# Kernel tuning notes

Hardware: AMD Instinct MI355X
Metric: run time of the kernel (lower is better)

Reference implementation:

```python
import jax, jax.numpy as jnp
import numpy as np

EPS = 1e-15


def _trace(t):
    return jnp.einsum('bii->b', t)


def _ortho_loss(ss, k):
    n = jnp.linalg.norm(ss, axis=(-1, -2), keepdims=True)
    diff = ss / n - jnp.eye(k, dtype=ss.dtype) / np.float32(np.sqrt(k))
    return jnp.mean(jnp.linalg.norm(diff, axis=(-1, -2)))


def _mincut_terms(s, adj):
    out_adj = jnp.einsum('bnk,bnm,bml->bkl', s, adj, s)
    d_flat = adj.sum(-1)  # degrees [B,N]
    num = _trace(out_adj)
    den = _trace(jnp.einsum('bnk,bn,bnl->bkl', s, d_flat, s)) + EPS
    return out_adj, num, den, d_flat


def dense_mincut_rewiring(x, adj, s, mask):
    k = s.shape[-1]  # 2
    m = mask[..., None].astype(x.dtype)
    s = jax.nn.softmax(s, axis=-1) * m
    _, num, den, _ = _mincut_terms(s, adj)
    mincut_loss = -jnp.mean(num / den)
    ortho_loss = _ortho_loss(jnp.einsum('bnk,bnl->bkl', s, s), k)
    # laplacian derivative of spectral gap wrt A_uv: (f_u - f_v)^2, f = soft bipartition
    f = s[..., 0]
    dlam = (f[:, :, None] - f[:, None, :]) ** 2
    return adj * (1.0 - dlam), mincut_loss, ortho_loss


def dense_CT_rewiring(x, adj, s, mask):
    k = s.shape[-1]
    m = mask[..., None].astype(x.dtype)
    s = jax.nn.softmax(s, axis=-1) * m
    d_flat = adj.sum(-1)
    sds = _trace(jnp.einsum('bnk,bn,bnl->bkl', s, d_flat, s))
    sas = _trace(jnp.einsum('bnk,bnm,bml->bkl', s, adj, s))
    den = _trace(jnp.einsum('bnk,bnl->bkl', s, s)) + EPS
    ct_loss = jnp.mean((sds - sas) / den)  # tr(Z^T L Z) / tr(Z^T Z)
    ortho_loss = _ortho_loss(jnp.einsum('bnk,bnl->bkl', s, s), k)
    # pairwise CT distances ||z_u - z_v|| / vol(G), sparsified by A
    sq = (s * s).sum(-1)
    d2 = sq[:, :, None] + sq[:, None, :] - 2.0 * jnp.einsum('bnk,bmk->bnm', s, s)
    ct_dist = jnp.sqrt(jnp.maximum(d2, 0.0) + 1e-12)
    vol = d_flat.sum(-1)
    new_adj = (ct_dist / (vol[:, None, None] + EPS)) * adj
    return new_adj, ct_loss, ortho_loss


def dense_mincut_pool(x, adj, s, mask):
    k = s.shape[-1]
    m = mask[..., None].astype(x.dtype)
    s = jax.nn.softmax(s, axis=-1) * m
    x = x * m
    out = jnp.einsum('bnk,bnf->bkf', s, x)
    out_adj, num, den, _ = _mincut_terms(s, adj)
    mincut_loss = -jnp.mean(num / den)
    ortho_loss = _ortho_loss(jnp.einsum('bnk,bnl->bkl', s, s), k)
    out_adj = out_adj * (1.0 - jnp.eye(k, dtype=adj.dtype))  # zero diagonal
    d = jnp.sqrt(out_adj.sum(-1)) + EPS  # [B,k]
    out_adj = out_adj / d[:, None, :] / d[:, :, None]
    return out, out_adj, mincut_loss, ortho_loss


def _dgc(x, adj, w_rel, b_rel, w_root):
    # DenseGraphConv(aggr='add'): lin_rel(A @ x) + lin_root(x)
    return jnp.matmul(adj, x) @ w_rel + b_rel + x @ w_root


def setup_inputs() -> dict:
    B, N, IN, H, KC, OUT, KMC = 16, 1024, 128, 32, 32, 10, 16
    keys = iter(jax.random.split(jax.random.key(0), 48))

    def lin(fin, fout):
        lim = float(1.0 / np.sqrt(fin))
        return (jax.random.uniform(next(keys), (fin, fout), jnp.float32, -lim, lim),
                jax.random.uniform(next(keys), (fout,), jnp.float32, -lim, lim))

    x = jax.random.normal(next(keys), (B, N, IN), jnp.float32)
    u = jax.random.uniform(next(keys), (B, N, N), jnp.float32)
    a = (u < 0.0156).astype(jnp.float32)  # avg degree ~16
    adj = jnp.maximum(a, jnp.swapaxes(a, 1, 2)) * (1.0 - jnp.eye(N, dtype=jnp.float32))
    mask = jnp.ones((B, N), dtype=bool)
    W1, b1 = lin(IN, H)
    Wrw, brw = lin(H, 2)
    Wg_rel, bg = lin(H, H); Wg_root, _ = lin(H, H)
    Wmcg, bmcg = lin(H, KMC)
    W2g_rel, b2g = lin(H, H); W2g_root, _ = lin(H, H)
    Wct, bct = lin(H, KC)
    Wc_rel, bc = lin(H, H); Wc_root, _ = lin(H, H)
    Wmcc, bmcc = lin(H, KMC)
    Wcat, bcat = lin(2 * H, H)
    W2, b2 = lin(H, H)
    W3, b3 = lin(H, OUT)
    return dict(x=x, adj=adj, mask=mask, W1=W1, b1=b1, Wrw=Wrw, brw=brw,
                Wg_rel=Wg_rel, bg=bg, Wg_root=Wg_root, Wmcg=Wmcg, bmcg=bmcg,
                W2g_rel=W2g_rel, b2g=b2g, W2g_root=W2g_root, Wct=Wct, bct=bct,
                Wc_rel=Wc_rel, bc=bc, Wc_root=Wc_root, Wmcc=Wmcc, bmcc=bmcc,
                Wcat=Wcat, bcat=bcat, W2=W2, b2=b2, W3=W3, b3=b3)


def reference(x, adj, mask, W1, b1, Wrw, brw, Wg_rel, bg, Wg_root, Wmcg, bmcg,
              W2g_rel, b2g, W2g_root, Wct, bct, Wc_rel, bc, Wc_root, Wmcc, bmcc,
              Wcat, bcat, W2, b2, W3, b3):
    x = x @ W1 + b1
    # GAP branch
    adj_gap, mc_rw, ol_rw = dense_mincut_rewiring(x, adj, x @ Wrw + brw, mask)
    x_gap = _dgc(x, adj_gap, Wg_rel, bg, Wg_root)
    x_gap, adj_gap, mc1, ol1 = dense_mincut_pool(x_gap, adj_gap, x_gap @ Wmcg + bmcg, mask)
    x_gap = _dgc(x_gap, adj_gap, W2g_rel, b2g, W2g_root)
    # CT branch
    adj_ct, ct_loss, ol_ct = dense_CT_rewiring(x, adj, x @ Wct + bct, mask)
    x_ct = _dgc(x, adj_ct, Wc_rel, bc, Wc_root)
    x_ct, adj_ct, mc2, ol2 = dense_mincut_pool(x_ct, adj_ct, x_ct @ Wmcc + bmcc, mask)
    x_ct = _dgc(x_ct, adj_ct, W2g_rel, b2g, W2g_root)  # source reuses self.conv2gap here
    h = jax.nn.relu(jnp.concatenate([x_gap, x_ct], axis=2) @ Wcat + bcat).sum(axis=1)
    h = jax.nn.relu(h @ W2 + b2)
    logits = h @ W3 + b3
    main_loss = mc_rw + ct_loss + mc1 + mc2
    ortho_loss = ol_rw + ol_ct + ol1 + ol2
    return (jax.nn.log_softmax(logits, axis=-1), main_loss, ortho_loss)
```

## Files before the change

### kernel.cpp

```cpp
#include <hip/hip_runtime.h>
#include <math.h>

#define BB   16
#define NNODE 1024
#define INF_ 128
#define HH   32
#define KMC  16
#define CAP  128
#define EPS15 1e-15f

typedef float v4f __attribute__((ext_vector_type(4)));

#define OFF_X      0
#define OFF_SRW    524288
#define OFF_SQCT   557056
#define OFF_SCT    573440
#define OFF_D      1097728
#define OFF_NUMRW  1114112
#define OFF_SAS    1130496
#define OFF_DGAP   1146880
#define OFF_DCT    1163264
#define OFF_XGAP   2228224
#define OFF_XCT    2752512
#define OFF_S2G    3276800
#define OFF_S2C    3538944
#define OFF_FROB   4325376
#define OFF_VOL    4325888
#define OFF_OUTG   4326032
#define OFF_OUTC   4334224
#define OFF_G2G    4342416
#define OFF_G2C    4346512
#define OFF_OAG    4350608
#define OFF_OAC    4354704
#define OFF_ENNZ   4358800
#define OFF_EIDX   4375184
#define OFF_EWG    5423760
#define OFF_EWC    7520912
#define OFF_PACK   9618064
#define OFF_BSUM   9683600

__device__ __forceinline__ float wave_sum(float v) {
#pragma unroll
  for (int off = 32; off >= 1; off >>= 1) v += __shfl_xor(v, off, 64);
  return v;
}

__device__ __forceinline__ void wave_sum4(float& a, float& b, float& c, float& d) {
#pragma unroll
  for (int off = 32; off >= 1; off >>= 1) {
    a += __shfl_xor(a, off, 64);
    b += __shfl_xor(b, off, 64);
    c += __shfl_xor(c, off, 64);
    d += __shfl_xor(d, off, 64);
  }
}

__device__ __forceinline__ void team_reduce_f4(float4& a) {
#pragma unroll
  for (int off = 4; off <= 32; off <<= 1) {
    a.x += __shfl_xor(a.x, off, 64);
    a.y += __shfl_xor(a.y, off, 64);
    a.z += __shfl_xor(a.z, off, 64);
    a.w += __shfl_xor(a.w, off, 64);
  }
}

__device__ __forceinline__ float blk_sum(float v, float* sred, int tid) {
  v = wave_sum(v);
  __syncthreads();
  if ((tid & 63) == 0) sred[tid >> 6] = v;
  __syncthreads();
  return sred[0] + sred[1] + sred[2] + sred[3];
}

__device__ __forceinline__ void blk_sum5(float* v, float (*sm)[4], int tid) {
  int w = tid >> 6, lane = tid & 63;
#pragma unroll
  for (int i = 0; i < 5; i++) {
#pragma unroll
    for (int off = 32; off >= 1; off >>= 1) v[i] += __shfl_xor(v[i], off, 64);
  }
  if (lane == 0) {
#pragma unroll
    for (int i = 0; i < 5; i++) sm[i][w] = v[i];
  }
  __syncthreads();
#pragma unroll
  for (int i = 0; i < 5; i++) v[i] = sm[i][0] + sm[i][1] + sm[i][2] + sm[i][3];
}

__global__ __launch_bounds__(256) void k_fused0(
    const float* __restrict__ adj, const float* __restrict__ x,
    const float* __restrict__ W1, const float* __restrict__ b1,
    const float* __restrict__ Wrw, const float* __restrict__ brw,
    const float* __restrict__ Wct, const float* __restrict__ bct,
    float* __restrict__ ws)
{
  __shared__ __align__(16) float sW1[INF_*HH];
  __shared__ __align__(16) float sWct[HH*HH];
  __shared__ float sWrw[HH*2];
  __shared__ float sb1[HH], sbct[HH], sbrw[2];
  __shared__ __align__(16) float sx[8*INF_];
  __shared__ float sX[8*HH];
  __shared__ unsigned int s_e32[4][4][CAP/2];
  int tid = threadIdx.x;
  if (blockIdx.x < 1024) {
    int w = tid >> 6, lane = tid & 63;
    int row0 = blockIdx.x * 16 + w * 4;
    v4f v[16];
#pragma unroll
    for (int rr = 0; rr < 4; rr++) {
      const v4f* ar = (const v4f*)(adj + (size_t)(row0 + rr) * NNODE);
#pragma unroll
      for (int it = 0; it < 4; it++)
        v[rr*4 + it] = __builtin_nontemporal_load(&ar[it*64 + lane]);
    }
#pragma unroll
    for (int rr = 0; rr < 4; rr++) {
      int row = row0 + rr;
      int c = 0;
#pragma unroll
      for (int it = 0; it < 4; it++) {
        v4f a4 = v[rr*4 + it];
        c += (a4.x != 0.f) + (a4.y != 0.f) + (a4.z != 0.f) + (a4.w != 0.f);
      }
      int p = c;
#pragma unroll
      for (int off = 1; off < 64; off <<= 1) {
        int t = __shfl_up(p, off, 64);
        if (lane >= off) p += t;
      }
      int excl = p - c;
      int total = __shfl(p, 63, 64);
      unsigned short* es = (unsigned short*)s_e32[w][rr];
      int pos = excl;
#pragma unroll
      for (int it = 0; it < 4; it++) {
        v4f a4 = v[rr*4 + it];
        int m0 = it*256 + lane*4;
        if (a4.x != 0.f) { if (pos < CAP) es[pos] = (unsigned short)(m0+0); pos++; }
        if (a4.y != 0.f) { if (pos < CAP) es[pos] = (unsigned short)(m0+1); pos++; }
        if (a4.z != 0.f) { if (pos < CAP) es[pos] = (unsigned short)(m0+2); pos++; }
        if (a4.w != 0.f) { if (pos < CAP) es[pos] = (unsigned short)(m0+3); pos++; }
      }
      int nnzc = total < CAP ? total : CAP;
      __syncthreads();
      unsigned int* dst = (unsigned int*)((unsigned short*)(ws + OFF_EIDX) + (size_t)row*CAP);
      int n32 = (nnzc + 1) >> 1;
      if (lane < n32) dst[lane] = s_e32[w][rr][lane];
      if (lane == 0) {
        ((int*)(ws + OFF_ENNZ))[row] = nnzc;
        ws[OFF_D + row] = (float)total;
      }
    }
  } else {
    for (int i = tid; i < INF_*HH/4; i += 256)
      ((float4*)sW1)[i] = ((const float4*)W1)[i];
    ((float4*)sWct)[tid] = ((const float4*)Wct)[tid];
    if (tid < HH*2) sWrw[tid] = Wrw[tid];
    if (tid < HH) { sb1[tid] = b1[tid]; sbct[tid] = bct[tid]; }
    if (tid < 2) sbrw[tid] = brw[tid];
    size_t row0 = (size_t)(blockIdx.x - 1024) * 8;
    ((float4*)sx)[tid] = ((const float4*)(x + row0 * INF_))[tid];
    __syncthreads();
    int r = tid >> 5, h = tid & 31;
    float acc = sb1[h];
#pragma unroll 8
    for (int k = 0; k < INF_; k++) acc += sx[r*INF_ + k] * sW1[k*HH + h];
    size_t row = row0 + r;
    ws[OFF_X + row*HH + h] = acc;
    sX[r*HH + h] = acc;
    __syncthreads();
    float sraw = sbct[h];
#pragma unroll
    for (int k = 0; k < HH; k++) sraw += sX[r*HH + k] * sWct[k*HH + h];
    float mx = sraw;
#pragma unroll
    for (int off = 16; off >= 1; off >>= 1) mx = fmaxf(mx, __shfl_xor(mx, off, 32));
    float e = __expf(sraw - mx);
    float sum = e;
#pragma unroll
    for (int off = 16; off >= 1; off >>= 1) sum += __shfl_xor(sum, off, 32);
    float sv = e / sum;
    ws[OFF_SCT + row*HH + h] = sv;
    float sq = sv * sv;
#pragma unroll
    for (int off = 16; off >= 1; off >>= 1) sq += __shfl_xor(sq, off, 32);
    float xv = sX[r*HH + h];
    float t0 = xv * sWrw[h*2 + 0];
    float t1 = xv * sWrw[h*2 + 1];
#pragma unroll
    for (int off = 16; off >= 1; off >>= 1) { t0 += __shfl_xor(t0, off, 32); t1 += __shfl_xor(t1, off, 32); }
    if (h == 0) {
      ws[OFF_SQCT + row] = sq;
      float r0 = t0 + sbrw[0], r1 = t1 + sbrw[1];
      float m2 = fmaxf(r0, r1);
      float e0 = __expf(r0 - m2), e1 = __expf(r1 - m2);
      float inv = 1.0f / (e0 + e1);
      float s0 = e0*inv, s1 = e1*inv;
      ((float2*)(ws + OFF_SRW))[row] = make_float2(s0, s1);
      ((float4*)(ws + OFF_PACK))[row] = make_float4(s0, s1, sq, 0.f);
    }
  }
}

__global__ __launch_bounds__(256) void k_edgefeat(
    const float* __restrict__ Wg_rel, const float* __restrict__ bg, const float* __restrict__ Wg_root,
    const float* __restrict__ Wc_rel, const float* __restrict__ bc, const float* __restrict__ Wc_root,
    const float* __restrict__ Wmcg, const float* __restrict__ bmcg,
    const float* __restrict__ Wmcc, const float* __restrict__ bmcc,
    float* __restrict__ out, float* __restrict__ ws)
{
  __shared__ float sp[8][32];
  __shared__ float sred[4];
  __shared__ __align__(16) float sWgrel[HH*HH], sWgroot[HH*HH], sWcrel[HH*HH], sWcroot[HH*HH];
  __shared__ float sbg[HH], sbc[HH];
  __shared__ __align__(16) float sYg[4*HH], sYc[4*HH];
  __shared__ float sXr[4*HH], sxg[4*HH], sxc[4*HH];
  int tid = threadIdx.x;
  if (blockIdx.x < 4096) {
    int xcd = blockIdx.x & 7;
    int idx = blockIdx.x >> 3;
    int b = xcd*2 + (idx >> 8);
    int chunk = idx & 255;
    int base4 = b*NNODE + chunk*4;
    ((float4*)sWgrel)[tid]  = ((const float4*)Wg_rel)[tid];
    ((float4*)sWgroot)[tid] = ((const float4*)Wg_root)[tid];
    ((float4*)sWcrel)[tid]  = ((const float4*)Wc_rel)[tid];
    ((float4*)sWcroot)[tid] = ((const float4*)Wc_root)[tid];
    if (tid < HH)  { sbg[tid] = bg[tid]; sbc[tid] = bc[tid]; }
    if (tid < 128) sXr[tid] = ws[OFF_X + (size_t)base4*HH + tid];
    float vp = 0.f;
#pragma unroll
    for (int i = 0; i < 4; i++) vp += ws[OFF_D + (size_t)b*NNODE + tid + i*256];

    const float* X = ws + OFF_X;
    const float2* srw = (const float2*)(ws + OFF_SRW);
    const float* sqct = ws + OFF_SQCT;
    const float* sct = ws + OFF_SCT;
    const float4* pack = (const float4*)(ws + OFF_PACK) + (size_t)b*NNODE;
    int w = tid >> 6, lane = tid & 63;
    int tm = lane & 3;
    int row = base4 + w;
    int nnz = ((const int*)(ws + OFF_ENNZ))[row];
    const unsigned short* eidx = (const unsigned short*)(ws + OFF_EIDX) + (size_t)row*CAP;
    const float4* cn4 = (const float4*)(sct + (size_t)row * HH);
    float4 c0 = cn4[tm*2], c1 = cn4[tm*2 + 1];
    float2 srwn = srw[row];
    float f_n = srwn.x;
    float sq_n = sqct[row];
    float numrw_p = 0.f, sas_p = 0.f, dg_p = 0.f, dc_p = 0.f;
    float4 yg0 = make_float4(0,0,0,0), yg1 = make_float4(0,0,0,0);
    float4 yc0 = make_float4(0,0,0,0), yc1 = make_float4(0,0,0,0);
    for (int e = (lane >> 2); e < nnz; e += 16) {
      int m = eidx[e];
      size_t mo = ((size_t)b*NNODE + m);
      const float4* cm4 = (const float4*)(sct + mo * HH);
      const float4* xm4 = (const float4*)(X + mo * HH);
      float4 d0 = cm4[tm*2], d1 = cm4[tm*2 + 1];
      float4 x0 = xm4[tm*2], x1 = xm4[tm*2 + 1];
      float4 pk = pack[m];
      float dot = c0.x*d0.x + c0.y*d0.y + c0.z*d0.z + c0.w*d0.w
                + c1.x*d1.x + c1.y*d1.y + c1.z*d1.z + c1.w*d1.w;
      dot += __shfl_xor(dot, 1, 64);
      dot += __shfl_xor(dot, 2, 64);
      numrw_p += srwn.x*pk.x + srwn.y*pk.y;
      float df = f_n - pk.x;
      float wg = 1.0f - df*df;
      float d2 = sq_n + pk.z - 2.0f*dot;
      float wc = sqrtf(fmaxf(d2, 0.0f) + 1e-12f);
      sas_p += dot;
      dg_p += wg;
      dc_p += wc;
      yg0.x += wg*x0.x; yg0.y += wg*x0.y; yg0.z += wg*x0.z; yg0.w += wg*x0.w;
      yg1.x += wg*x1.x; yg1.y += wg*x1.y; yg1.z += wg*x1.z; yg1.w += wg*x1.w;
      yc0.x += wc*x0.x; yc0.y += wc*x0.y; yc0.z += wc*x0.z; yc0.w += wc*x0.w;
      yc1.x += wc*x1.x; yc1.y += wc*x1.y; yc1.z += wc*x1.z; yc1.w += wc*x1.w;
      if (tm == 0) {
        size_t eo = (size_t)row*CAP + e;
        ws[OFF_EWG + eo] = wg;
        ws[OFF_EWC + eo] = wc;
      }
    }
    wave_sum4(numrw_p, sas_p, dg_p, dc_p);
    if (lane == 0) {
      ws[OFF_NUMRW + row] = numrw_p * 0.25f;
      ws[OFF_SAS + row] = sas_p * 0.25f;
      ws[OFF_DGAP + row] = dg_p * 0.25f;
      ws[OFF_DCT + row] = dc_p * 0.25f;
    }
    team_reduce_f4(yg0); team_reduce_f4(yg1);
    team_reduce_f4(yc0); team_reduce_f4(yc1);
    if (lane < 4) {
      ((float4*)&sYg[w*HH + tm*8])[0] = yg0;
      ((float4*)&sYg[w*HH + tm*8])[1] = yg1;
      ((float4*)&sYc[w*HH + tm*8])[0] = yc0;
      ((float4*)&sYc[w*HH + tm*8])[1] = yc1;
    }
    float vol = blk_sum(vp, sred, tid);
    float ivol = 1.0f / (vol + EPS15);
    {
      int r = tid >> 6;
      int h = (tid >> 1) & 31;
      int half = tid & 1;
      int kb = half * 16;
      float accg = 0.f, accg2 = 0.f, accc = 0.f, accc2 = 0.f;
#pragma unroll
      for (int kk = 0; kk < 16; kk++) {
        int k = kb + kk;
        float ygv = sYg[r*HH + k], Xv = sXr[r*HH + k], ycv = sYc[r*HH + k];
        accg  += ygv * sWgrel[k*HH + h];
        accg2 += Xv  * sWgroot[k*HH + h];
        accc  += ycv * sWcrel[k*HH + h];
        accc2 += Xv  * sWcroot[k*HH + h];
      }
      accg  += __shfl_xor(accg, 1, 64);
      accg2 += __shfl_xor(accg2, 1, 64);
      accc  += __shfl_xor(accc, 1, 64);
      accc2 += __shfl_xor(accc2, 1, 64);
      if (half == 0) {
        float xgv = sbg[h] + accg + accg2;
        float xcv = sbc[h] + ivol*accc + accc2;
        size_t rw = (size_t)base4 + r;
        ws[OFF_XGAP + rw*HH + h] = xgv;
        ws[OFF_XCT  + rw*HH + h] = xcv;
        sxg[r*HH + h] = xgv;
        sxc[r*HH + h] = xcv;
      }
    }
    __syncthreads();
    if (tid < 128) {
      int r = tid >> 5, h = tid & 31;
      int j = h & 15, halfsel = h >> 4;
      const float* sin_ = halfsel ? sxc : sxg;
      const float* sw = halfsel ? Wmcc : Wmcg;
      float raw = halfsel ? bmcc[j] : bmcg[j];
#pragma unroll
      for (int k = 0; k < HH; k++) raw += sin_[r*HH + k] * sw[k*KMC + j];
      float mx = raw;
#pragma unroll
      for (int off = 8; off >= 1; off >>= 1) mx = fmaxf(mx, __shfl_xor(mx, off, 16));
      float e = __expf(raw - mx);
      float sum = e;
#pragma unroll
      for (int off = 8; off >= 1; off >>= 1) sum += __shfl_xor(sum, off, 16);
      float sv = e / sum;
      size_t rw = (size_t)base4 + r;
      if (halfsel == 0) ws[OFF_S2G + rw*KMC + j] = sv;
      else              ws[OFF_S2C + rw*KMC + j] = sv;
    }
  } else if (blockIdx.x < 4608) {
    int blk = blockIdx.x - 4096;
    int xcd = blk & 7;
    int idx = blk >> 3;
    int b = xcd*2 + (idx >> 5);
    int i = idx & 31;
    const float* sct = ws + OFF_SCT + (size_t)b*NNODE*HH;
    int j = tid & 31, seg = tid >> 5;
    float acc = 0.f;
    for (int n = seg*128; n < seg*128 + 128; n++)
      acc += sct[n*HH + i] * sct[n*HH + j];
    sp[seg][j] = acc;
    __syncthreads();
    if (tid < 32) {
      float g = 0.f;
#pragma unroll
      for (int s = 0; s < 8; s++) g += sp[s][tid];
      float p = g * g;
#pragma unroll
      for (int off = 16; off >= 1; off >>= 1) p += __shfl_xor(p, off, 32);
      if (tid == 0) ws[OFF_FROB + b*32 + i] = p;
    }
  } else {
    int b = blockIdx.x - 4608;
    if (b == 0 && tid < 2) out[160 + tid] = 0.f;
    if (tid < 12) ws[OFF_BSUM + b*12 + tid] = 0.f;
    for (int i = tid; i < 2048; i += 256) ws[OFF_OUTG + b*2048 + i] = 0.f;
    float vp = 0.f;
    for (int n = tid; n < NNODE; n += 256) vp += ws[OFF_D + (size_t)b*NNODE + n];
    float vol = blk_sum(vp, sred, tid);
    if (tid == 0) ws[OFF_VOL + b] = vol;
  }
}

__global__ __launch_bounds__(512) void k_passred(float* __restrict__ ws)
{
  __shared__ float sg[32*16], sc[32*16], stg[32*16], stc[32*16];
  __shared__ float sxg[32*32], sxc[32*32];
  int xcd = blockIdx.x & 7;
  int idx = blockIdx.x >> 3;
  int b = xcd*2 + (idx >> 5);
  int chunk = idx & 31;
  int tid = threadIdx.x;
  size_t n0 = (size_t)b * NNODE + chunk * 32;
  const float* pG  = ws + OFF_S2G  + n0 * KMC;
  const float* pC  = ws + OFF_S2C  + n0 * KMC;
  const float* pXG = ws + OFF_XGAP + n0 * HH;
  const float* pXC = ws + OFF_XCT  + n0 * HH;
  sg[tid] = pG[tid];
  sc[tid] = pC[tid];
  sxg[tid] = pXG[tid]; sxg[tid + 512] = pXG[tid + 512];
  sxc[tid] = pXC[tid]; sxc[tid + 512] = pXC[tid + 512];
  {
    int r = tid >> 4, k = tid & 15;
    size_t row = n0 + r;
    int nnz = ((const int*)(ws + OFF_ENNZ))[row];
    const unsigned short* eidx = (const unsigned short*)(ws + OFF_EIDX) + row * CAP;
    const float* ewg = ws + OFF_EWG + row * CAP;
    const float* ewc = ws + OFF_EWC + row * CAP;
    const float* S2G = ws + OFF_S2G + (size_t)b * NNODE * KMC;
    const float* S2C = ws + OFF_S2C + (size_t)b * NNODE * KMC;
    float ag = 0.f, ac = 0.f;
    int e = 0;
    for (; e + 1 < nnz; e += 2) {
      int m0 = eidx[e], m1 = eidx[e + 1];
      float g0 = ewg[e], g1 = ewg[e + 1];
      float c0 = ewc[e], c1 = ewc[e + 1];
      ag += g0 * S2G[(size_t)m0 * KMC + k] + g1 * S2G[(size_t)m1 * KMC + k];
      ac += c0 * S2C[(size_t)m0 * KMC + k] + c1 * S2C[(size_t)m1 * KMC + k];
    }
    if (e < nnz) {
      int m = eidx[e];
      ag += ewg[e] * S2G[(size_t)m * KMC + k];
      ac += ewc[e] * S2C[(size_t)m * KMC + k];
    }
    stg[r * 16 + k] = ag;
    stc[r * 16 + k] = ac;
  }
  __syncthreads();
  int sub = tid >> 8, t = tid & 255;
  { int k0 = t >> 5, h0 = t & 31;
    float og0 = 0.f, og1 = 0.f, oc0 = 0.f, oc1 = 0.f;
#pragma unroll
    for (int i = 0; i < 16; i++) {
      int r = sub * 16 + i;
      float xgv = sxg[r*32 + h0], xcv = sxc[r*32 + h0];
      og0 += sg[r*16 + k0]     * xgv;
      og1 += sg[r*16 + k0 + 8] * xgv;
      oc0 += sc[r*16 + k0]     * xcv;
      oc1 += sc[r*16 + k0 + 8] * xcv;
    }
    atomicAdd(&ws[OFF_OUTG + b*512 + k0*32 + h0],     og0);
    atomicAdd(&ws[OFF_OUTG + b*512 + (k0+8)*32 + h0], og1);
    atomicAdd(&ws[OFF_OUTC + b*512 + k0*32 + h0],     oc0);
    atomicAdd(&ws[OFF_OUTC + b*512 + (k0+8)*32 + h0], oc1);
  }
  { int kk = t >> 4, l = t & 15;
    float gg = 0.f, gc = 0.f, ag = 0.f, ac = 0.f;
#pragma unroll
    for (int i = 0; i < 16; i++) {
      int r = sub * 16 + i;
      float sgk = sg[r*16 + kk], sck = sc[r*16 + kk];
      gg += sgk * sg [r*16 + l];
      gc += sck * sc [r*16 + l];
      ag += sgk * stg[r*16 + l];
      ac += sck * stc[r*16 + l];
    }
    atomicAdd(&ws[OFF_G2G + b*256 + t], gg);
    atomicAdd(&ws[OFF_G2C + b*256 + t], gc);
    atomicAdd(&ws[OFF_OAG + b*256 + t], ag);
    atomicAdd(&ws[OFF_OAC + b*256 + t], ac);
  }
  if (tid < 32) {
    size_t gn = n0 + tid;
    float ng = 0.f, nc = 0.f;
#pragma unroll
    for (int j = 0; j < KMC; j++) {
      float a = sg[tid*16 + j], c2 = sc[tid*16 + j];
      ng += a*a; nc += c2*c2;
    }
    float dgv = ws[OFF_DGAP + gn];
    float dcv = ws[OFF_DCT + gn];
    float d   = ws[OFF_D + gn];
    float2 s  = ((const float2*)(ws + OFF_SRW))[gn];
    float sq  = ws[OFF_SQCT + gn];
    float nmr = ws[OFF_NUMRW + gn];
    float sasv= ws[OFF_SAS + gn];
    float u0 = dgv*ng, u1 = dcv*nc, u2 = ng, u3 = nc;
    float u4 = d*(s.x*s.x + s.y*s.y), u5 = nmr, u6 = d*sq, u7 = sasv;
    float u8 = sq, u9 = s.x*s.x, u10 = s.x*s.y, u11 = s.y*s.y;
#pragma unroll
    for (int off = 16; off >= 1; off >>= 1) {
      u0 += __shfl_xor(u0, off, 32);  u1 += __shfl_xor(u1, off, 32);
      u2 += __shfl_xor(u2, off, 32);  u3 += __shfl_xor(u3, off, 32);
      u4 += __shfl_xor(u4, off, 32);  u5 += __shfl_xor(u5, off, 32);
      u6 += __shfl_xor(u6, off, 32);  u7 += __shfl_xor(u7, off, 32);
      u8 += __shfl_xor(u8, off, 32);  u9 += __shfl_xor(u9, off, 32);
      u10 += __shfl_xor(u10, off, 32); u11 += __shfl_xor(u11, off, 32);
    }
    if (tid == 0) {
      float* bs = ws + OFF_BSUM + b*12;
      atomicAdd(bs + 0, u0);  atomicAdd(bs + 1, u1);  atomicAdd(bs + 2, u2);
      atomicAdd(bs + 3, u3);  atomicAdd(bs + 4, u4);  atomicAdd(bs + 5, u5);
      atomicAdd(bs + 6, u6);  atomicAdd(bs + 7, u7);  atomicAdd(bs + 8, u8);
      atomicAdd(bs + 9, u9);  atomicAdd(bs + 10, u10); atomicAdd(bs + 11, u11);
    }
  }
}

__global__ __launch_bounds__(256) void k_batch2(
    const float* __restrict__ W2g_rel, const float* __restrict__ b2g, const float* __restrict__ W2g_root,
    const float* __restrict__ Wcat, const float* __restrict__ bcat,
    const float* __restrict__ W2, const float* __restrict__ b2,
    const float* __restrict__ W3, const float* __restrict__ b3,
    float* __restrict__ out, float* __restrict__ ws)
{
  __shared__ float sOAg[256], sOAc[256], sOutg[512], sOutc[512];
  __shared__ float sW2grel[1024], sW2groot[1024], sWcat[2048], sW2l[1024];
  __shared__ float sPg[512], sPc[512], sXg2[512], sXc2[512], sHt[512];
  __shared__ float sHs[32], sH2[32], sLg[16], sScal[2];
  __shared__ float sdkg[16], sdkc[16];
  __shared__ float smm[5][4];
  int b = blockIdx.x, tid = threadIdx.x;
  sOAg[tid] = ws[OFF_OAG + b*256 + tid];
  sOAc[tid] = ws[OFF_OAC + b*256 + tid];
  sOutg[tid]       = ws[OFF_OUTG + b*512 + tid];
  sOutg[tid + 256] = ws[OFF_OUTG + b*512 + tid + 256];
  sOutc[tid]       = ws[OFF_OUTC + b*512 + tid];
  sOutc[tid + 256] = ws[OFF_OUTC + b*512 + tid + 256];
  for (int i = tid; i < 1024; i += 256) { sW2grel[i] = W2g_rel[i]; sW2groot[i] = W2g_root[i]; sW2l[i] = W2[i]; }
  for (int i = tid; i < 2048; i += 256) sWcat[i] = Wcat[i];
  float v[5];
  v[0] = (tid < 32) ? ws[OFF_FROB + b*32 + tid] : 0.f;
  float gv = ws[OFF_G2G + b*256 + tid];
  float cv = ws[OFF_G2C + b*256 + tid];
  v[1] = gv*gv; v[2] = cv*cv;
  __syncthreads();
  v[3] = (tid < 16) ? sOAg[tid*17] : 0.f;
  v[4] = (tid < 16) ? sOAc[tid*17] : 0.f;
  blk_sum5(v, smm, tid);
  float frob2 = v[0], frobg2 = v[1], frobc2 = v[2], num1 = v[3], num2u = v[4];
  float vol = ws[OFF_VOL + b];
  float ivol = 1.0f / (vol + EPS15);
  if (tid == 0) {
    const float* bs = ws + OFF_BSUM + b*12;
    float den1 = bs[0], den2u = bs[1], trg = bs[2], trc = bs[3];
    float denrw = bs[4], num = bs[5], sds = bs[6], sas = bs[7], denct = bs[8];
    float g00 = bs[9], g01 = bs[10], g11 = bs[11];
    float mcrw = -num / (denrw + EPS15);
    float ctb  = (sds - sas) / (denct + EPS15);
    float nrw = sqrtf(g00*g00 + 2.f*g01*g01 + g11*g11);
    float olrw = sqrtf(fmaxf(2.f - 2.f*(g00 + g11)/(nrw*1.41421356237f), 0.f));
    float nct = sqrtf(frob2);
    float olct = sqrtf(fmaxf(2.f - 2.f*denct/(nct*5.65685424949f), 0.f));
    float mc1 = -num1 / (den1 + EPS15);
    float mc2 = -(num2u*ivol) / (den2u*ivol + EPS15);
    float ol1 = sqrtf(fmaxf(2.f - 2.f*trg/(sqrtf(frobg2)*4.f), 0.f));
    float ol2 = sqrtf(fmaxf(2.f - 2.f*trc/(sqrtf(frobc2)*4.f), 0.f));
    atomicAdd(out + 160, (mcrw + ctb + mc1 + mc2) * 0.0625f);
    atomicAdd(out + 161, (olrw + olct + ol1 + ol2) * 0.0625f);
  }
  sOAc[tid] *= ivol;
  __syncthreads();
  if (tid < 16) { sOAg[tid*17] = 0.f; sOAc[tid*17] = 0.f; }
  __syncthreads();
  if (tid < 16) {
    float rg = 0.f, rc = 0.f;
#pragma unroll
    for (int l = 0; l < 16; l++) { rg += sOAg[tid*16 + l]; rc += sOAc[tid*16 + l]; }
    sdkg[tid] = sqrtf(rg) + EPS15;
    sdkc[tid] = sqrtf(rc) + EPS15;
  }
  __syncthreads();
  { int k = tid >> 4, l = tid & 15;
    sOAg[tid] /= (sdkg[k]*sdkg[l]);
    sOAc[tid] /= (sdkc[k]*sdkc[l]); }
  __syncthreads();
  { int k = tid >> 5, h = tid & 31;
    float p0 = 0, p1 = 0, q0 = 0, q1 = 0;
#pragma unroll
    for (int l = 0; l < 16; l++) {
      p0 += sOAg[k*16 + l] * sOutg[l*32 + h];
      p1 += sOAg[(k+8)*16 + l] * sOutg[l*32 + h];
      q0 += sOAc[k*16 + l] * sOutc[l*32 + h];
      q1 += sOAc[(k+8)*16 + l] * sOutc[l*32 + h];
    }
    sPg[k*32 + h] = p0; sPg[(k+8)*32 + h] = p1;
    sPc[k*32 + h] = q0; sPc[(k+8)*32 + h] = q1;
  }
  __syncthreads();
  { int k = tid >> 5, h = tid & 31;
    float bb2 = b2g[h];
    float a0 = bb2, a1 = bb2, c0 = bb2, c1 = bb2;
#pragma unroll
    for (int q = 0; q < 32; q++) {
      float wr = sW2grel[q*32 + h], wo = sW2groot[q*32 + h];
      a0 += sPg[k*32 + q]*wr + sOutg[k*32 + q]*wo;
      a1 += sPg[(k+8)*32 + q]*wr + sOutg[(k+8)*32 + q]*wo;
      c0 += sPc[k*32 + q]*wr + sOutc[k*32 + q]*wo;
      c1 += sPc[(k+8)*32 + q]*wr + sOutc[(k+8)*32 + q]*wo;
    }
    sXg2[k*32 + h] = a0; sXg2[(k+8)*32 + h] = a1;
    sXc2[k*32 + h] = c0; sXc2[(k+8)*32 + h] = c1;
  }
  __syncthreads();
  { int k = tid >> 5, h = tid & 31;
    float bb = bcat[h];
    float t0 = bb, t1 = bb;
#pragma unroll
    for (int q = 0; q < 32; q++) {
      float w1v = sWcat[q*32 + h], w2v = sWcat[(q+32)*32 + h];
      t0 += sXg2[k*32 + q]*w1v + sXc2[k*32 + q]*w2v;
      t1 += sXg2[(k+8)*32 + q]*w1v + sXc2[(k+8)*32 + q]*w2v;
    }
    sHt[k*32 + h] = fmaxf(t0, 0.f);
    sHt[(k+8)*32 + h] = fmaxf(t1, 0.f);
  }
  __syncthreads();
  if (tid < 32) {
    float s = 0.f;
#pragma unroll
    for (int k = 0; k < 16; k++) s += sHt[k*32 + tid];
    sHs[tid] = s;
  }
  __syncthreads();
  if (tid < 32) {
    float a = b2[tid];
#pragma unroll
    for (int q = 0; q < 32; q++) a += sHs[q]*sW2l[q*32 + tid];
    sH2[tid] = fmaxf(a, 0.f);
  }
  __syncthreads();
  if (tid < 10) {
    float a = b3[tid];
#pragma unroll
    for (int q = 0; q < 32; q++) a += sH2[q]*W3[q*10 + tid];
    sLg[tid] = a;
  }
  __syncthreads();
  if (tid == 0) {
    float m = sLg[0];
    for (int o = 1; o < 10; o++) m = fmaxf(m, sLg[o]);
    float se = 0.f;
    for (int o = 0; o < 10; o++) se += __expf(sLg[o] - m);
    sScal[0] = m; sScal[1] = logf(se);
  }
  __syncthreads();
  if (tid < 10) out[b*10 + tid] = sLg[tid] - sScal[0] - sScal[1];
}

extern "C" void kernel_launch(void* const* d_in, const int* in_sizes, int n_in,
                              void* d_out, int out_size, void* d_ws, size_t ws_size,
                              hipStream_t stream)
{
  const float* x       = (const float*)d_in[0];
  const float* adj     = (const float*)d_in[1];
  const float* W1      = (const float*)d_in[3];
  const float* b1      = (const float*)d_in[4];
  const float* Wrw     = (const float*)d_in[5];
  const float* brw     = (const float*)d_in[6];
  const float* Wg_rel  = (const float*)d_in[7];
  const float* bg      = (const float*)d_in[8];
  const float* Wg_root = (const float*)d_in[9];
  const float* Wmcg    = (const float*)d_in[10];
  const float* bmcg    = (const float*)d_in[11];
  const float* W2g_rel = (const float*)d_in[12];
  const float* b2g     = (const float*)d_in[13];
  const float* W2g_root= (const float*)d_in[14];
  const float* Wct     = (const float*)d_in[15];
  const float* bct     = (const float*)d_in[16];
  const float* Wc_rel  = (const float*)d_in[17];
  const float* bc      = (const float*)d_in[18];
  const float* Wc_root = (const float*)d_in[19];
  const float* Wmcc    = (const float*)d_in[20];
  const float* bmcc    = (const float*)d_in[21];
  const float* Wcat    = (const float*)d_in[22];
  const float* bcat    = (const float*)d_in[23];
  const float* W2      = (const float*)d_in[24];
  const float* b2      = (const float*)d_in[25];
  const float* W3      = (const float*)d_in[26];
  const float* b3      = (const float*)d_in[27];
  float* out = (float*)d_out;
  float* ws  = (float*)d_ws;

  k_fused0<<<dim3(3072), dim3(256), 0, stream>>>(adj, x, W1, b1, Wrw, brw, Wct, bct, ws);
  k_edgefeat<<<dim3(4624), dim3(256), 0, stream>>>(Wg_rel, bg, Wg_root, Wc_rel, bc, Wc_root,
                                                   Wmcg, bmcg, Wmcc, bmcc, out, ws);
  k_passred<<<dim3(512), dim3(512), 0, stream>>>(ws);
  k_batch2<<<dim3(16), dim3(256), 0, stream>>>(W2g_rel, b2g, W2g_root, Wcat, bcat,
                                               W2, b2, W3, b3, out, ws);
}
```

Baseline: 248.0 us.

## Process four rows per wave in edge-feature kernel, drop shared weight staging

The edge-feature kernel now has each wave loop over four rows, so a block covers 16 rows and the grid shrinks from 4096 to 1024 blocks for that part. The per-block staging of four 32x32 weight matrices into shared memory and the block-wide volume reduction are removed. Weights are read directly from global or L2, the volume is reduced per wave, and the dense projection and softmax run wave-locally without block barriers. This amortizes per-block setup and synchronization, at the cost of fewer blocks, less parallelism and repeated uncached global weight reads.

```diff
diff --git a/kernel.cpp b/kernel.cpp
--- a/kernel.cpp
+++ b/kernel.cpp
@@ -213,144 +213,141 @@
 {
   __shared__ float sp[8][32];
   __shared__ float sred[4];
-  __shared__ __align__(16) float sWgrel[HH*HH], sWgroot[HH*HH], sWcrel[HH*HH], sWcroot[HH*HH];
-  __shared__ float sbg[HH], sbc[HH];
-  __shared__ __align__(16) float sYg[4*HH], sYc[4*HH];
-  __shared__ float sXr[4*HH], sxg[4*HH], sxc[4*HH];
+  __shared__ __align__(16) float sY[4][2][HH];
+  __shared__ __align__(16) float sXw[4][HH];
+  __shared__ float sxgw[4][HH], sxcw[4][HH];
   int tid = threadIdx.x;
-  if (blockIdx.x < 4096) {
+  if (blockIdx.x < 1024) {
     int xcd = blockIdx.x & 7;
     int idx = blockIdx.x >> 3;
-    int b = xcd*2 + (idx >> 8);
-    int chunk = idx & 255;
-    int base4 = b*NNODE + chunk*4;
-    ((float4*)sWgrel)[tid]  = ((const float4*)Wg_rel)[tid];
-    ((float4*)sWgroot)[tid] = ((const float4*)Wg_root)[tid];
-    ((float4*)sWcrel)[tid]  = ((const float4*)Wc_rel)[tid];
-    ((float4*)sWcroot)[tid] = ((const float4*)Wc_root)[tid];
-    if (tid < HH)  { sbg[tid] = bg[tid]; sbc[tid] = bc[tid]; }
-    if (tid < 128) sXr[tid] = ws[OFF_X + (size_t)base4*HH + tid];
-    float vp = 0.f;
-#pragma unroll
-    for (int i = 0; i < 4; i++) vp += ws[OFF_D + (size_t)b*NNODE + tid + i*256];
-
+    int b = xcd*2 + (idx >> 6);
+    int chunk = idx & 63;
+    int base16 = b*NNODE + chunk*16;
+    int w = tid >> 6, lane = tid & 63;
+    int tm = lane & 3;
+    int h = lane & 31, half = lane >> 5;
+    int j = lane & 15, gsel = (lane >> 4) & 1;
     const float* X = ws + OFF_X;
+    const float* sct = ws + OFF_SCT;
     const float2* srw = (const float2*)(ws + OFF_SRW);
     const float* sqct = ws + OFF_SQCT;
-    const float* sct = ws + OFF_SCT;
     const float4* pack = (const float4*)(ws + OFF_PACK) + (size_t)b*NNODE;
-    int w = tid >> 6, lane = tid & 63;
-    int tm = lane & 3;
-    int row = base4 + w;
-    int nnz = ((const int*)(ws + OFF_ENNZ))[row];
-    const unsigned short* eidx = (const unsigned short*)(ws + OFF_EIDX) + (size_t)row*CAP;
-    const float4* cn4 = (const float4*)(sct + (size_t)row * HH);
-    float4 c0 = cn4[tm*2], c1 = cn4[tm*2 + 1];
-    float2 srwn = srw[row];
-    float f_n = srwn.x;
-    float sq_n = sqct[row];
-    float numrw_p = 0.f, sas_p = 0.f, dg_p = 0.f, dc_p = 0.f;
-    float4 yg0 = make_float4(0,0,0,0), yg1 = make_float4(0,0,0,0);
-    float4 yc0 = make_float4(0,0,0,0), yc1 = make_float4(0,0,0,0);
-    for (int e = (lane >> 2); e < nnz; e += 16) {
-      int m = eidx[e];
-      size_t mo = ((size_t)b*NNODE + m);
-      const float4* cm4 = (const float4*)(sct + mo * HH);
-      const float4* xm4 = (const float4*)(X + mo * HH);
-      float4 d0 = cm4[tm*2], d1 = cm4[tm*2 + 1];
-      float4 x0 = xm4[tm*2], x1 = xm4[tm*2 + 1];
-      float4 pk = pack[m];
-      float dot = c0.x*d0.x + c0.y*d0.y + c0.z*d0.z + c0.w*d0.w
-                + c1.x*d1.x + c1.y*d1.y + c1.z*d1.z + c1.w*d1.w;
-      dot += __shfl_xor(dot, 1, 64);
-      dot += __shfl_xor(dot, 2, 64);
-      numrw_p += srwn.x*pk.x + srwn.y*pk.y;
-      float df = f_n - pk.x;
-      float wg = 1.0f - df*df;
-      float d2 = sq_n + pk.z - 2.0f*dot;
-      float wc = sqrtf(fmaxf(d2, 0.0f) + 1e-12f);
-      sas_p += dot;
-      dg_p += wg;
-      dc_p += wc;
-      yg0.x += wg*x0.x; yg0.y += wg*x0.y; yg0.z += wg*x0.z; yg0.w += wg*x0.w;
-      yg1.x += wg*x1.x; yg1.y += wg*x1.y; yg1.z += wg*x1.z; yg1.w += wg*x1.w;
-      yc0.x += wc*x0.x; yc0.y += wc*x0.y; yc0.z += wc*x0.z; yc0.w += wc*x0.w;
-      yc1.x += wc*x1.x; yc1.y += wc*x1.y; yc1.z += wc*x1.z; yc1.w += wc*x1.w;
-      if (tm == 0) {
-        size_t eo = (size_t)row*CAP + e;
-        ws[OFF_EWG + eo] = wg;
-        ws[OFF_EWC + eo] = wc;
-      }
-    }
-    wave_sum4(numrw_p, sas_p, dg_p, dc_p);
-    if (lane == 0) {
-      ws[OFF_NUMRW + row] = numrw_p * 0.25f;
-      ws[OFF_SAS + row] = sas_p * 0.25f;
-      ws[OFF_DGAP + row] = dg_p * 0.25f;
-      ws[OFF_DCT + row] = dc_p * 0.25f;
-    }
-    team_reduce_f4(yg0); team_reduce_f4(yg1);
-    team_reduce_f4(yc0); team_reduce_f4(yc1);
-    if (lane < 4) {
-      ((float4*)&sYg[w*HH + tm*8])[0] = yg0;
-      ((float4*)&sYg[w*HH + tm*8])[1] = yg1;
-      ((float4*)&sYc[w*HH + tm*8])[0] = yc0;
-      ((float4*)&sYc[w*HH + tm*8])[1] = yc1;
-    }
-    float vol = blk_sum(vp, sred, tid);
-    float ivol = 1.0f / (vol + EPS15);
-    {
-      int r = tid >> 6;
-      int h = (tid >> 1) & 31;
-      int half = tid & 1;
-      int kb = half * 16;
-      float accg = 0.f, accg2 = 0.f, accc = 0.f, accc2 = 0.f;
-#pragma unroll
-      for (int kk = 0; kk < 16; kk++) {
-        int k = kb + kk;
-        float ygv = sYg[r*HH + k], Xv = sXr[r*HH + k], ycv = sYc[r*HH + k];
-        accg  += ygv * sWgrel[k*HH + h];
-        accg2 += Xv  * sWgroot[k*HH + h];
-        accc  += ycv * sWcrel[k*HH + h];
-        accc2 += Xv  * sWcroot[k*HH + h];
-      }
-      accg  += __shfl_xor(accg, 1, 64);
-      accg2 += __shfl_xor(accg2, 1, 64);
-      accc  += __shfl_xor(accc, 1, 64);
-      accc2 += __shfl_xor(accc2, 1, 64);
-      if (half == 0) {
-        float xgv = sbg[h] + accg + accg2;
-        float xcv = sbc[h] + ivol*accc + accc2;
-        size_t rw = (size_t)base4 + r;
-        ws[OFF_XGAP + rw*HH + h] = xgv;
-        ws[OFF_XCT  + rw*HH + h] = xcv;
-        sxg[r*HH + h] = xgv;
-        sxc[r*HH + h] = xcv;
-      }
-    }
-    __syncthreads();
-    if (tid < 128) {
-      int r = tid >> 5, h = tid & 31;
-      int j = h & 15, halfsel = h >> 4;
-      const float* sin_ = halfsel ? sxc : sxg;
-      const float* sw = halfsel ? Wmcc : Wmcg;
-      float raw = halfsel ? bmcc[j] : bmcg[j];
-#pragma unroll
-      for (int k = 0; k < HH; k++) raw += sin_[r*HH + k] * sw[k*KMC + j];
-      float mx = raw;
-#pragma unroll
-      for (int off = 8; off >= 1; off >>= 1) mx = fmaxf(mx, __shfl_xor(mx, off, 16));
-      float e = __expf(raw - mx);
-      float sum = e;
-#pragma unroll
-      for (int off = 8; off >= 1; off >>= 1) sum += __shfl_xor(sum, off, 16);
-      float sv = e / sum;
-      size_t rw = (size_t)base4 + r;
-      if (halfsel == 0) ws[OFF_S2G + rw*KMC + j] = sv;
-      else              ws[OFF_S2C + rw*KMC + j] = sv;
-    }
-  } else if (blockIdx.x < 4608) {
-    int blk = blockIdx.x - 4096;
+    float bgv = bg[h], bcv = bc[h];
+    float bmv = gsel ? bmcc[j] : bmcg[j];
+    const float* Wmc = gsel ? Wmcc : Wmcg;
+    float vp = 0.f;
+#pragma unroll
+    for (int i = 0; i < 16; i++) vp += ws[OFF_D + (size_t)b*NNODE + lane + i*64];
+    float ivol = 1.0f / (wave_sum(vp) + EPS15);
+
+    for (int rr = 0; rr < 4; rr++) {
+      int row = base16 + w*4 + rr;
+      int nnz = ((const int*)(ws + OFF_ENNZ))[row];
+      const unsigned short* eidx = (const unsigned short*)(ws + OFF_EIDX) + (size_t)row*CAP;
+      const float4* cn4 = (const float4*)(sct + (size_t)row * HH);
+      float4 c0 = cn4[tm*2], c1 = cn4[tm*2 + 1];
+      if (lane < 8) ((float4*)sXw[w])[lane] = ((const float4*)(X + (size_t)row * HH))[lane];
+      float2 srwn = srw[row];
+      float f_n = srwn.x;
+      float sq_n = sqct[row];
+      float numrw_p = 0.f, sas_p = 0.f, dg_p = 0.f, dc_p = 0.f;
+      float4 yg0 = make_float4(0,0,0,0), yg1 = make_float4(0,0,0,0);
+      float4 yc0 = make_float4(0,0,0,0), yc1 = make_float4(0,0,0,0);
+      for (int e = (lane >> 2); e < nnz; e += 16) {
+        int m = eidx[e];
+        size_t mo = ((size_t)b*NNODE + m);
+        const float4* cm4 = (const float4*)(sct + mo * HH);
+        const float4* xm4 = (const float4*)(X + mo * HH);
+        float4 d0 = cm4[tm*2], d1 = cm4[tm*2 + 1];
+        float4 x0 = xm4[tm*2], x1 = xm4[tm*2 + 1];
+        float4 pk = pack[m];
+        float dot = c0.x*d0.x + c0.y*d0.y + c0.z*d0.z + c0.w*d0.w
+                  + c1.x*d1.x + c1.y*d1.y + c1.z*d1.z + c1.w*d1.w;
+        dot += __shfl_xor(dot, 1, 64);
+        dot += __shfl_xor(dot, 2, 64);
+        numrw_p += srwn.x*pk.x + srwn.y*pk.y;
+        float df = f_n - pk.x;
+        float wg = 1.0f - df*df;
+        float d2 = sq_n + pk.z - 2.0f*dot;
+        float wc = sqrtf(fmaxf(d2, 0.0f) + 1e-12f);
+        sas_p += dot;
+        dg_p += wg;
+        dc_p += wc;
+        yg0.x += wg*x0.x; yg0.y += wg*x0.y; yg0.z += wg*x0.z; yg0.w += wg*x0.w;
+        yg1.x += wg*x1.x; yg1.y += wg*x1.y; yg1.z += wg*x1.z; yg1.w += wg*x1.w;
+        yc0.x += wc*x0.x; yc0.y += wc*x0.y; yc0.z += wc*x0.z; yc0.w += wc*x0.w;
+        yc1.x += wc*x1.x; yc1.y += wc*x1.y; yc1.z += wc*x1.z; yc1.w += wc*x1.w;
+        if (tm == 0) {
+          size_t eo = (size_t)row*CAP + e;
+          ws[OFF_EWG + eo] = wg;
+          ws[OFF_EWC + eo] = wc;
+        }
+      }
+      wave_sum4(numrw_p, sas_p, dg_p, dc_p);
+      if (lane == 0) {
+        ws[OFF_NUMRW + row] = numrw_p * 0.25f;
+        ws[OFF_SAS + row] = sas_p * 0.25f;
+        ws[OFF_DGAP + row] = dg_p * 0.25f;
+        ws[OFF_DCT + row] = dc_p * 0.25f;
+      }
+      team_reduce_f4(yg0); team_reduce_f4(yg1);
+      team_reduce_f4(yc0); team_reduce_f4(yc1);
+      if (lane < 4) {
+        ((float4*)&sY[w][0][tm*8])[0] = yg0;
+        ((float4*)&sY[w][0][tm*8])[1] = yg1;
+        ((float4*)&sY[w][1][tm*8])[0] = yc0;
+        ((float4*)&sY[w][1][tm*8])[1] = yc1;
+      }
+      {
+        float accg = 0.f, accg2 = 0.f, accc = 0.f, accc2 = 0.f;
+#pragma unroll
+        for (int kk = 0; kk < 16; kk++) {
+          int k = half*16 + kk;
+          float ygv = sY[w][0][k], Xv = sXw[w][k], ycv = sY[w][1][k];
+          accg  += ygv * Wg_rel[k*HH + h];
+          accg2 += Xv  * Wg_root[k*HH + h];
+          accc  += ycv * Wc_rel[k*HH + h];
+          accc2 += Xv  * Wc_root[k*HH + h];
+        }
+        accg  += __shfl_xor(accg, 32, 64);
+        accg2 += __shfl_xor(accg2, 32, 64);
+        accc  += __shfl_xor(accc, 32, 64);
+        accc2 += __shfl_xor(accc2, 32, 64);
+        float xgv = bgv + accg + accg2;
+        float xcv = bcv + ivol*accc + accc2;
+        if (half == 0) {
+          ws[OFF_XGAP + (size_t)row*HH + h] = xgv;
+          ws[OFF_XCT  + (size_t)row*HH + h] = xcv;
+          sxgw[w][h] = xgv;
+          sxcw[w][h] = xcv;
+        }
+      }
+      {
+        const float* xin = gsel ? sxcw[w] : sxgw[w];
+        float raw = 0.f;
+#pragma unroll
+        for (int kk = 0; kk < 16; kk++) {
+          int k = half*16 + kk;
+          raw += xin[k] * Wmc[k*KMC + j];
+        }
+        raw += __shfl_xor(raw, 32, 64);
+        raw += bmv;
+        float mx = raw;
+#pragma unroll
+        for (int off = 8; off >= 1; off >>= 1) mx = fmaxf(mx, __shfl_xor(mx, off, 64));
+        float e = __expf(raw - mx);
+        float sum = e;
+#pragma unroll
+        for (int off = 8; off >= 1; off >>= 1) sum += __shfl_xor(sum, off, 64);
+        float sv = e / sum;
+        if (half == 0) {
+          if (gsel == 0) ws[OFF_S2G + (size_t)row*KMC + j] = sv;
+          else           ws[OFF_S2C + (size_t)row*KMC + j] = sv;
+        }
+      }
+    }
+  } else if (blockIdx.x < 1536) {
+    int blk = blockIdx.x - 1024;
     int xcd = blk & 7;
     int idx = blk >> 3;
     int b = xcd*2 + (idx >> 5);
@@ -372,7 +369,7 @@
       if (tid == 0) ws[OFF_FROB + b*32 + i] = p;
     }
   } else {
-    int b = blockIdx.x - 4608;
+    int b = blockIdx.x - 1536;
     if (b == 0 && tid < 2) out[160 + tid] = 0.f;
     if (tid < 12) ws[OFF_BSUM + b*12 + tid] = 0.f;
     for (int i = tid; i < 2048; i += 256) ws[OFF_OUTG + b*2048 + i] = 0.f;
@@ -674,7 +671,7 @@
   float* ws  = (float*)d_ws;
 
   k_fused0<<<dim3(3072), dim3(256), 0, stream>>>(adj, x, W1, b1, Wrw, brw, Wct, bct, ws);
-  k_edgefeat<<<dim3(4624), dim3(256), 0, stream>>>(Wg_rel, bg, Wg_root, Wc_rel, bc, Wc_root,
+  k_edgefeat<<<dim3(1552), dim3(256), 0, stream>>>(Wg_rel, bg, Wg_root, Wc_rel, bc, Wc_root,
                                                    Wmcg, bmcg, Wmcc, bmcc, out, ws);
   k_passred<<<dim3(512), dim3(512), 0, stream>>>(ws);
   k_batch2<<<dim3(16), dim3(256), 0, stream>>>(W2g_rel, b2g, W2g_root, Wcat, bcat,
```

Measured after the change: 253.3 us. 2.1% more time.
